# Optimization experiments

Hardware: AMD Instinct MI355X
Metric: run time of the kernel (lower is better)

Reference implementation:

```python
import jax, jax.numpy as jnp
import numpy as np

B, L, D = 8, 512, 256


def hard_sigmoid(x):
    # Keras 1.x default inner_activation for LSTM gates
    return jnp.clip(0.2 * x + 0.5, 0.0, 1.0)


def lstm_step(x_t, h, c, W, U, b):
    # gates in Keras order: i, f, g(candidate), o
    z = x_t @ W + h @ U + b  # (B, 4D)
    i, f, g, o = jnp.split(z, 4, axis=-1)
    i = hard_sigmoid(i)
    f = hard_sigmoid(f)
    g = jnp.tanh(g)
    o = hard_sigmoid(o)
    c_new = f * c + i * g
    h_new = o * jnp.tanh(c_new)
    return h_new, c_new


def setup_inputs() -> dict:
    key = jax.random.key(0)
    ks = jax.random.split(key, 10)
    s = 1.0 / np.sqrt(D)
    x = jax.random.normal(ks[0], (B, L, D), dtype=jnp.float32)
    W_r = jax.random.normal(ks[1], (D, 4 * D), dtype=jnp.float32) * s
    U_r = jax.random.normal(ks[2], (D, 4 * D), dtype=jnp.float32) * s
    b_r = jnp.zeros((4 * D,), dtype=jnp.float32)
    W_w = jax.random.normal(ks[3], (D, 4 * D), dtype=jnp.float32) * s
    U_w = jax.random.normal(ks[4], (D, 4 * D), dtype=jnp.float32) * s
    b_w = jnp.zeros((4 * D,), dtype=jnp.float32)
    W_c = jax.random.normal(ks[5], (2 * D, D), dtype=jnp.float32) * s
    b_c = jnp.zeros((D,), dtype=jnp.float32)
    return {"x": x, "W_r": W_r, "U_r": U_r, "b_r": b_r,
            "W_w": W_w, "U_w": U_w, "b_w": b_w, "W_c": W_c, "b_c": b_c}


def reference(x, W_r, U_r, b_r, W_w, U_w, b_w, W_c, b_c):
    Bb, Ll, Dd = x.shape
    h0 = jnp.zeros((Bb, Dd), dtype=x.dtype)

    # --- reader LSTM (return_sequences=True), eq. 1 ---
    def reader_step(carry, x_t):
        h, c = carry
        h, c = lstm_step(x_t, h, c, W_r, U_r, b_r)
        return (h, c), h

    _, o_seq = jax.lax.scan(reader_step, (h0, h0), jnp.swapaxes(x, 0, 1))  # (L, B, D)

    # --- compose-and-write loop, eqs. 2-6; mem_0 = x ---
    def write_step(carry, o_t):
        mem, h, c = carry  # mem: (B, L, D)
        z = jax.nn.softmax(jnp.einsum('bd,bld->bl', o_t, mem), axis=-1)  # (B, L)
        m_rt = jnp.einsum('bl,bld->bd', z, mem)                           # (B, D)
        c_t = jnp.concatenate([o_t, m_rt], axis=-1) @ W_c + b_c          # linear composer
        h_new, c_new = lstm_step(c_t, h, c, W_w, U_w, b_w)
        mem_new = mem * (1.0 - z[..., None]) + h_new[:, None, :] * z[..., None]
        return (mem_new, h_new, c_new), h_new

    (_, _, _), h_seq = jax.lax.scan(write_step, (x, h0, h0), o_seq)
    # return_mode == 'last_output'
    return h_seq[-1]
```

## Files before the change

kernel.cpp:

```cpp
#include <hip/hip_runtime.h>
#include <math.h>

#define BB 8
#define LL 512
#define DD 256
#define NG4 1024
#define WGB 32
#define WR 16
#define WU 8
#define MLD 264

typedef __attribute__((ext_vector_type(4))) float f32x4;
typedef __attribute__((ext_vector_type(2))) unsigned u32x2;
typedef __attribute__((ext_vector_type(4))) unsigned u32x4;

static const size_t OFF_XW    = 0;
static const size_t OFF_F     = OFF_XW + (size_t)BB*LL*NG4;
static const size_t OFF_BMW   = OFF_F + (size_t)DD*NG4;
static const size_t OFF_B2    = OFF_BMW + (size_t)DD*NG4;
static const size_t OFF_HRT   = OFF_B2 + NG4;
static const size_t OFF_HWT   = OFF_HRT + (size_t)2*BB*DD*2;
static const size_t OFF_RHOT  = OFF_HWT + (size_t)BB*DD*2;
static const size_t OFF_CHUNK = OFF_RHOT + (size_t)BB*WGB*2;
static const size_t OFF_PM    = OFF_CHUNK + (size_t)BB*WGB*4;
static const size_t TOTAL_WS  = OFF_PM + (size_t)BB*WGB*DD;

__device__ __forceinline__ float hsig(float x) {
    return fminf(fmaxf(0.2f*x + 0.5f, 0.0f), 1.0f);
}

__device__ __forceinline__ void st_coh(float* p, float v) {
    __hip_atomic_store(p, v, __ATOMIC_RELAXED, __HIP_MEMORY_SCOPE_AGENT);
}
__device__ __forceinline__ void st_pair(unsigned* p, float v, unsigned tag) {
    u32x2 d; d[0] = __float_as_uint(v); d[1] = tag;
    asm volatile("global_store_dwordx2 %0, %1, off sc0 sc1" :: "v"(p), "v"(d) : "memory");
}
__device__ __forceinline__ u32x2 ld_pair(const unsigned* p) {
    u32x2 r;
    asm volatile("global_load_dwordx2 %0, %1, off sc0 sc1\n\ts_waitcnt vmcnt(0)"
                 : "=&v"(r) : "v"(p) : "memory");
    return r;
}
__device__ __forceinline__ float poll_pair(const unsigned* p, unsigned tag) {
    for (;;) {
        u32x2 r = ld_pair(p);
        if (r[1] >= tag) return __uint_as_float(r[0]);
    }
}
__device__ __forceinline__ u32x4 ld_chunk(const unsigned* p) {
    u32x4 r;
    asm volatile("global_load_dwordx4 %0, %1, off sc0 sc1\n\ts_waitcnt vmcnt(0)"
                 : "=&v"(r) : "v"(p) : "memory");
    return r;
}
__device__ __forceinline__ void ld_pm8(
    const f32x4* p0, const f32x4* p1, const f32x4* p2, const f32x4* p3,
    const f32x4* p4, const f32x4* p5, const f32x4* p6, const f32x4* p7,
    f32x4& a0, f32x4& a1, f32x4& a2, f32x4& a3,
    f32x4& a4, f32x4& a5, f32x4& a6, f32x4& a7)
{
    asm volatile(
        "global_load_dwordx4 %0, %8, off sc0 sc1\n\t"
        "global_load_dwordx4 %1, %9, off sc0 sc1\n\t"
        "global_load_dwordx4 %2, %10, off sc0 sc1\n\t"
        "global_load_dwordx4 %3, %11, off sc0 sc1\n\t"
        "global_load_dwordx4 %4, %12, off sc0 sc1\n\t"
        "global_load_dwordx4 %5, %13, off sc0 sc1\n\t"
        "global_load_dwordx4 %6, %14, off sc0 sc1\n\t"
        "global_load_dwordx4 %7, %15, off sc0 sc1\n\t"
        "s_waitcnt vmcnt(0)"
        : "=&v"(a0), "=&v"(a1), "=&v"(a2), "=&v"(a3),
          "=&v"(a4), "=&v"(a5), "=&v"(a6), "=&v"(a7)
        : "v"(p0), "v"(p1), "v"(p2), "v"(p3),
          "v"(p4), "v"(p5), "v"(p6), "v"(p7)
        : "memory");
}

template<int TM, int TN, int TK>
__global__ void __launch_bounds__(256) gemm_nn(
    const float* __restrict__ A, int lda,
    const float* __restrict__ Bmat, int ldb,
    const float* __restrict__ bias,
    float* __restrict__ C, int ldc,
    int M, int N, int K)
{
    __shared__ float As[TK][TM];
    __shared__ float Bs[TK][TN];
    const int m0 = blockIdx.y * TM, n0 = blockIdx.x * TN;
    const int tid = threadIdx.x;
    const int tx = tid % (TN/4);
    const int ty = tid / (TN/4);
    float acc[4][4] = {};
    for (int k0 = 0; k0 < K; k0 += TK) {
        {
            const int e = tid*4;
            const int m = e / TK, k = e % TK;
            const float4 v = *reinterpret_cast<const float4*>(&A[(size_t)(m0+m)*lda + k0 + k]);
            As[k+0][m] = v.x; As[k+1][m] = v.y; As[k+2][m] = v.z; As[k+3][m] = v.w;
        }
        {
            const int e = tid*4;
            const int k = e / TN, n = e % TN;
            const float4 v = *reinterpret_cast<const float4*>(&Bmat[(size_t)(k0+k)*ldb + n0 + n]);
            Bs[k][n+0] = v.x; Bs[k][n+1] = v.y; Bs[k][n+2] = v.z; Bs[k][n+3] = v.w;
        }
        __syncthreads();
        #pragma unroll
        for (int kk = 0; kk < TK; ++kk) {
            float a[4], bv[4];
            #pragma unroll
            for (int i = 0; i < 4; ++i) a[i] = As[kk][ty*4+i];
            #pragma unroll
            for (int j = 0; j < 4; ++j) bv[j] = Bs[kk][tx*4+j];
            #pragma unroll
            for (int i = 0; i < 4; ++i)
                #pragma unroll
                for (int j = 0; j < 4; ++j) acc[i][j] += a[i]*bv[j];
        }
        __syncthreads();
    }
    #pragma unroll
    for (int i = 0; i < 4; ++i) {
        const int m = m0 + ty*4 + i;
        #pragma unroll
        for (int j = 0; j < 4; ++j) {
            const int n = n0 + tx*4 + j;
            C[(size_t)m*ldc + n] = acc[i][j] + (bias ? bias[n] : 0.0f);
        }
    }
}

__global__ void __launch_bounds__(256) b2_kernel(
    const float* __restrict__ bc, const float* __restrict__ Ww,
    const float* __restrict__ bw, float* __restrict__ B2)
{
    const int n = blockIdx.x*256 + threadIdx.x;
    float a = bw[n];
    for (int k = 0; k < DD; ++k) a += bc[k]*Ww[(size_t)k*NG4 + n];
    B2[n] = a;
}

__global__ void __launch_bounds__(256) fused_kernel(
    const float* __restrict__ XW, const float* __restrict__ Fw,
    const float* __restrict__ Bm, const float* __restrict__ B2,
    const float* __restrict__ Ur, const float* __restrict__ Uw,
    const float* __restrict__ x,
    unsigned* __restrict__ HRT, unsigned* __restrict__ HWT,
    unsigned* __restrict__ RHOT, unsigned* __restrict__ CHUNK,
    float* __restrict__ PM, float* __restrict__ out)
{
    extern __shared__ float sm[];
    float* Urs  = sm;
    float* Uws  = Urs + 8192;
    float* Fs   = Uws + 8192;
    float* Bms  = Fs + 8192;
    float* mems = Bms + 8192;
    float* hr2  = mems + WR*MLD;
    float* hw   = hr2 + 512;
    float* ms   = hw + 256;
    float* zredR= ms + 256;
    float* zredW= zredR + 256;
    float* red4 = zredW + 256;
    float* xws  = red4 + 1024;
    float* b2s  = xws + 32;
    float* zrs  = b2s + 32;
    float* zws  = zrs + 32;
    float* fwS  = zws + 32;
    float* d1   = fwS + 32;
    float* zp   = d1 + 16;
    float* esx  = zp + 16;
    float* wv   = esx + 16;
    float* cr   = wv + 16;
    float* cw   = cr + 8;
    float* misc = cw + 8;

    const int b   = (int)blockIdx.x & 7;
    const int wg  = (int)blockIdx.x >> 3;
    const int tid = threadIdx.x;
    const int R0  = wg*WR;
    const int U0  = wg*WU;
    const int gc32 = (tid>>3)*DD + U0 + (tid&7);

    for (int it = 0; it < 32; ++it) {
        const int e = it*256 + tid;
        const int k = e >> 5, cl = e & 31;
        const int gc = (cl>>3)*DD + U0 + (cl&7);
        Urs[k*32+cl] = Ur[(size_t)k*NG4 + gc];
        Uws[k*32+cl] = Uw[(size_t)k*NG4 + gc];
        Fs [k*32+cl] = Fw[(size_t)k*NG4 + gc];
        Bms[k*32+cl] = Bm[(size_t)k*NG4 + gc];
    }
    if (tid < 32) b2s[tid] = B2[gc32];
    for (int r = 0; r < WR; ++r)
        mems[r*MLD + tid] = x[((size_t)b*LL + R0 + r)*DD + tid];
    {
        const size_t base = (size_t)b*LL*NG4;
        const float zi = XW[base + tid];
        const float zg = XW[base + 512 + tid];
        const float zo = XW[base + 768 + tid];
        const float c0 = hsig(zi)*tanhf(zg);
        hr2[tid] = hsig(zo)*tanhf(c0);
        hr2[256 + tid] = 0.f;
        if (tid >= U0 && tid < U0+WU) cr[tid-U0] = c0;
    }
    if (tid < 16) { zp[tid] = 0.f; d1[tid] = 0.f; esx[tid] = 0.f; }
    if (tid < 8)  cw[tid] = 0.f;
    if (tid < 4)  misc[tid] = 0.f;
    __syncthreads();

    for (int s = 0; s <= LL; ++s) {
        const bool doW = (s >= 1);
        float* hrN_s = hr2 + (s&1)*256;
        float* hrO_s = hr2 + ((s+1)&1)*256;

        if (s <= LL-2 && tid < 32)
            xws[tid] = XW[((size_t)b*LL + s + 1)*NG4 + gc32];

        float hw_r = 0.f, rho_r = 0.f;
        if (s >= 2) {
            hw_r = poll_pair(HWT + 2*((size_t)b*DD + tid), (unsigned)(s-1));
            if (tid < 32)
                rho_r = poll_pair(RHOT + 2*(b*WGB + tid), (unsigned)(s-1));
        }
        hw[tid] = hw_r;
        __syncthreads();

        float ck_m = 0.f, ck_s = 0.f;
        if (tid < 32) {
            float d2 = rho_r;
            #pragma unroll
            for (int off = 16; off; off >>= 1) d2 += __shfl_xor(d2, off, 32);
            if (doW && tid < 16) {
                const float zpv = zp[tid];
                const float sc  = (1.f - zpv)*d1[tid] + zpv*d2;
                float m = sc;
                #pragma unroll
                for (int off = 8; off; off >>= 1) m = fmaxf(m, __shfl_xor(m, off, 16));
                const float e = __expf(sc - m);
                esx[tid] = e;
                wv[tid]  = e*(1.f - zpv);
                float sum = e, bp = e*zpv;
                #pragma unroll
                for (int off = 8; off; off >>= 1) {
                    sum += __shfl_xor(sum, off, 16);
                    bp  += __shfl_xor(bp,  off, 16);
                }
                if (tid == 0) { misc[2] = bp; ck_m = m; ck_s = sum; }
            }
        }
        __syncthreads();

        if (doW) {
            float p = misc[2]*hw_r;
            #pragma unroll
            for (int r = 0; r < WR; ++r) p += wv[r]*mems[r*MLD + tid];
            st_coh(&PM[((size_t)b*WGB + wg)*DD + tid], p);
        }
        asm volatile("s_waitcnt vmcnt(0)" ::: "memory");
        __syncthreads();
        if (doW && tid == 0) {
            u32x4 d; d[0] = __float_as_uint(ck_m); d[1] = __float_as_uint(ck_s);
            d[2] = (unsigned)s; d[3] = 0u;
            unsigned* cp = CHUNK + 4*(b*WGB + wg);
            asm volatile("global_store_dwordx4 %0, %1, off sc0 sc1" :: "v"(cp), "v"(d) : "memory");
        }
        if (s >= 2) {
            #pragma unroll
            for (int r = 0; r < WR; ++r) {
                const float z = zp[r];
                float* mp = &mems[r*MLD + tid];
                *mp = *mp*(1.f - z) + hw_r*z;
            }
        }
        if (doW) {
            const int kc = tid >> 5, cl = tid & 31, k0 = kc*32;
            float a = 0.f;
            #pragma unroll 8
            for (int k = k0; k < k0+32; ++k)
                a += hw[k]*Uws[k*32+cl] + hrO_s[k]*Fs[k*32+cl];
            zredW[tid] = a;
        }

        float hrN_r = 0.f;
        if (s >= 1 && s <= LL-1)
            hrN_r = poll_pair(HRT + 2*(((size_t)(s&1)*BB + b)*DD + tid), (unsigned)s);
        float pmx_r = 0.f, ps_r = 0.f;
        if (doW && tid < 32) {
            const unsigned* cp = CHUNK + 4*(b*WGB + tid);
            u32x4 ck;
            do { ck = ld_chunk(cp); } while (ck[2] < (unsigned)s);
            pmx_r = __uint_as_float(ck[0]); ps_r = __uint_as_float(ck[1]);
        }
        if (s >= 1 && s <= LL-1) hrN_s[tid] = hrN_r;
        __syncthreads();

        f32x4 a0={},a1={},a2={},a3={},a4={},a5={},a6={},a7={};
        const int w0 = tid >> 6, dq = tid & 63;
        if (doW) {
            const float* pmb = PM + (size_t)b*WGB*DD;
            ld_pm8((const f32x4*)(pmb + (w0+ 0)*DD) + dq, (const f32x4*)(pmb + (w0+ 4)*DD) + dq,
                   (const f32x4*)(pmb + (w0+ 8)*DD) + dq, (const f32x4*)(pmb + (w0+12)*DD) + dq,
                   (const f32x4*)(pmb + (w0+16)*DD) + dq, (const f32x4*)(pmb + (w0+20)*DD) + dq,
                   (const f32x4*)(pmb + (w0+24)*DD) + dq, (const f32x4*)(pmb + (w0+28)*DD) + dq,
                   a0,a1,a2,a3,a4,a5,a6,a7);
        }
        if (doW && tid < 32) {
            float g = pmx_r;
            #pragma unroll
            for (int off = 16; off; off >>= 1) g = fmaxf(g, __shfl_xor(g, off, 32));
            const float fw = __expf(pmx_r - g);
            float S = ps_r*fw;
            #pragma unroll
            for (int off = 16; off; off >>= 1) S += __shfl_xor(S, off, 32);
            fwS[tid] = fw;
            if (tid == 0)  misc[1] = 1.f/S;
            if (tid == wg) misc[0] = fw/S;
        }
        if (s <= LL-2) {
            const int kc = tid >> 5, cl = tid & 31, k0 = kc*32;
            float a = 0.f;
            #pragma unroll 8
            for (int k = k0; k < k0+32; ++k) a += hrN_s[k]*Urs[k*32+cl];
            zredR[tid] = a;
        }
        __syncthreads();

        if (doW) {
            f32x4 acc = a0*fwS[w0];
            acc += a1*fwS[w0+4];  acc += a2*fwS[w0+8];
            acc += a3*fwS[w0+12]; acc += a4*fwS[w0+16];
            acc += a5*fwS[w0+20]; acc += a6*fwS[w0+24];
            acc += a7*fwS[w0+28];
            *(f32x4*)(red4 + w0*DD + dq*4) = acc;
        }
        __syncthreads();
        if (doW) {
            ms[tid] = (red4[tid] + red4[DD+tid] + red4[2*DD+tid] + red4[3*DD+tid]) * misc[1];
            if (tid < 16) zp[tid] = esx[tid]*misc[0];
        }
        __syncthreads();
        if (doW) {
            const int kc = tid >> 5, cl = tid & 31, k0 = kc*32;
            float a = zredW[tid];
            #pragma unroll 8
            for (int k = k0; k < k0+32; ++k) a += ms[k]*Bms[k*32+cl];
            zredW[tid] = a;
        }
        __syncthreads();
        if (tid < 32) {
            if (doW) {
                float z = b2s[tid];
                #pragma unroll
                for (int q = 0; q < 8; ++q) z += zredW[q*32 + tid];
                zws[tid] = z;
            }
            if (s <= LL-2) {
                float z = xws[tid];
                #pragma unroll
                for (int q = 0; q < 8; ++q) z += zredR[q*32 + tid];
                zrs[tid] = z;
            }
        }
        __syncthreads();

        if (doW && tid < 8) {
            const float ig = hsig(zws[tid]);
            const float fg = hsig(zws[8+tid]);
            const float gg = tanhf(zws[16+tid]);
            const float og = hsig(zws[24+tid]);
            const float c  = fg*cw[tid] + ig*gg;
            cw[tid] = c;
            const float h = og*tanhf(c);
            st_pair(HWT + 2*((size_t)b*DD + U0 + tid), h, (unsigned)s);
            if (s < LL) {
                float rr = h * hrN_s[U0 + tid];
                rr += __shfl_down(rr, 4, 8);
                rr += __shfl_down(rr, 2, 8);
                rr += __shfl_down(rr, 1, 8);
                if (tid == 0) st_pair(RHOT + 2*(b*WGB + wg), rr, (unsigned)s);
            }
            if (s == LL) out[b*DD + U0 + tid] = h;
        }
        if (s <= LL-2 && tid < 8) {
            const float ig = hsig(zrs[tid]);
            const float fg = hsig(zrs[8+tid]);
            const float gg = tanhf(zrs[16+tid]);
            const float og = hsig(zrs[24+tid]);
            const float c  = fg*cr[tid] + ig*gg;
            cr[tid] = c;
            st_pair(HRT + 2*(((size_t)((s+1)&1)*BB + b)*DD + U0 + tid),
                    og*tanhf(c), (unsigned)(s+1));
        }
        if (s < LL) {
            const int r = tid >> 4, j = tid & 15;
            float a = 0.f;
            const float* mrow = mems + r*MLD;
            #pragma unroll 4
            for (int d = j; d < DD; d += 16) a += hrN_s[d]*mrow[d];
            #pragma unroll
            for (int off = 8; off; off >>= 1) a += __shfl_down(a, off, 16);
            if (j == 0) d1[r] = a;
        }
    }
}

extern "C" void kernel_launch(void* const* d_in, const int* in_sizes, int n_in,
                              void* d_out, int out_size, void* d_ws, size_t ws_size,
                              hipStream_t stream) {
    const float* x   = (const float*)d_in[0];
    const float* W_r = (const float*)d_in[1];
    const float* U_r = (const float*)d_in[2];
    const float* b_r = (const float*)d_in[3];
    const float* W_w = (const float*)d_in[4];
    const float* U_w = (const float*)d_in[5];
    const float* b_w = (const float*)d_in[6];
    const float* W_c = (const float*)d_in[7];
    const float* b_c = (const float*)d_in[8];
    (void)in_sizes; (void)n_in;

    if (ws_size < TOTAL_WS * sizeof(float)) return;

    float* ws   = (float*)d_ws;
    float* XW   = ws + OFF_XW;
    float* Fmat = ws + OFF_F;
    float* Bmw  = ws + OFF_BMW;
    float* B2   = ws + OFF_B2;
    unsigned* HRT   = (unsigned*)(ws + OFF_HRT);
    unsigned* HWT   = (unsigned*)(ws + OFF_HWT);
    unsigned* RHOT  = (unsigned*)(ws + OFF_RHOT);
    unsigned* CHUNK = (unsigned*)(ws + OFF_CHUNK);
    float* PM   = ws + OFF_PM;

    const int FUSED_LDS = 39800 * 4;
    hipFuncSetAttribute((const void*)fused_kernel, hipFuncAttributeMaxDynamicSharedMemorySize, FUSED_LDS);

    hipMemsetAsync(HRT, 0, (OFF_PM - OFF_HRT)*sizeof(float), stream);

    dim3 blk(256);
    gemm_nn<64,64,16><<<dim3(NG4/64, (BB*LL)/64), blk, 0, stream>>>(
        x, DD, W_r, NG4, b_r, XW, NG4, BB*LL, NG4, DD);
    gemm_nn<64,64,16><<<dim3(NG4/64, DD/64), blk, 0, stream>>>(
        W_c, DD, W_w, NG4, nullptr, Fmat, NG4, DD, NG4, DD);
    gemm_nn<64,64,16><<<dim3(NG4/64, DD/64), blk, 0, stream>>>(
        W_c + (size_t)DD*DD, DD, W_w, NG4, nullptr, Bmw, NG4, DD, NG4, DD);
    b2_kernel<<<dim3(NG4/256), blk, 0, stream>>>(b_c, W_w, b_w, B2);
    fused_kernel<<<dim3(BB*WGB), blk, FUSED_LDS, stream>>>(
        XW, Fmat, Bmw, B2, U_r, U_w, x, HRT, HWT, RHOT, CHUNK, PM, (float*)d_out);
}
```

Baseline: 3.784 ms.

## Tag partial-memory vectors per element to drop a barrier and reorder HW polling

Each partial memory-read value now goes out as a (value, step tag) pair, so consumers poll the tags directly and the producer no longer needs a vmcnt wait and barrier before publishing its chunk record. The hw-dependent term (bp·hw) is moved out of the per-workgroup partial into the consumer, using a bp value carried in the chunk record. That lets the HWT poll move later, overlapping the wait with the partial computation, and HWT is double-buffered by step parity. The cost is twice the traffic for partial reads, spin loops over 16 vector loads, and an extra barrier at the end of each step.

```diff
diff --git a/kernel.cpp b/kernel.cpp
--- a/kernel.cpp
+++ b/kernel.cpp
@@ -20,18 +20,15 @@
 static const size_t OFF_B2    = OFF_BMW + (size_t)DD*NG4;
 static const size_t OFF_HRT   = OFF_B2 + NG4;
 static const size_t OFF_HWT   = OFF_HRT + (size_t)2*BB*DD*2;
-static const size_t OFF_RHOT  = OFF_HWT + (size_t)BB*DD*2;
+static const size_t OFF_RHOT  = OFF_HWT + (size_t)2*BB*DD*2;
 static const size_t OFF_CHUNK = OFF_RHOT + (size_t)BB*WGB*2;
-static const size_t OFF_PM    = OFF_CHUNK + (size_t)BB*WGB*4;
-static const size_t TOTAL_WS  = OFF_PM + (size_t)BB*WGB*DD;
+static const size_t OFF_PMT   = OFF_CHUNK + (size_t)BB*WGB*4;
+static const size_t TOTAL_WS  = OFF_PMT + (size_t)BB*WGB*DD*2;
 
 __device__ __forceinline__ float hsig(float x) {
     return fminf(fmaxf(0.2f*x + 0.5f, 0.0f), 1.0f);
 }
 
-__device__ __forceinline__ void st_coh(float* p, float v) {
-    __hip_atomic_store(p, v, __ATOMIC_RELAXED, __HIP_MEMORY_SCOPE_AGENT);
-}
 __device__ __forceinline__ void st_pair(unsigned* p, float v, unsigned tag) {
     u32x2 d; d[0] = __float_as_uint(v); d[1] = tag;
     asm volatile("global_store_dwordx2 %0, %1, off sc0 sc1" :: "v"(p), "v"(d) : "memory");
@@ -54,26 +51,39 @@
                  : "=&v"(r) : "v"(p) : "memory");
     return r;
 }
-__device__ __forceinline__ void ld_pm8(
-    const f32x4* p0, const f32x4* p1, const f32x4* p2, const f32x4* p3,
-    const f32x4* p4, const f32x4* p5, const f32x4* p6, const f32x4* p7,
-    f32x4& a0, f32x4& a1, f32x4& a2, f32x4& a3,
-    f32x4& a4, f32x4& a5, f32x4& a6, f32x4& a7)
+
+__device__ __forceinline__ void ld_pmt16(
+    const unsigned* q0, const unsigned* q1, const unsigned* q2, const unsigned* q3,
+    const unsigned* q4, const unsigned* q5, const unsigned* q6, const unsigned* q7,
+    u32x4& A0, u32x4& B0, u32x4& A1, u32x4& B1,
+    u32x4& A2, u32x4& B2, u32x4& A3, u32x4& B3,
+    u32x4& A4, u32x4& B4, u32x4& A5, u32x4& B5,
+    u32x4& A6, u32x4& B6, u32x4& A7, u32x4& B7)
 {
     asm volatile(
-        "global_load_dwordx4 %0, %8, off sc0 sc1\n\t"
-        "global_load_dwordx4 %1, %9, off sc0 sc1\n\t"
-        "global_load_dwordx4 %2, %10, off sc0 sc1\n\t"
-        "global_load_dwordx4 %3, %11, off sc0 sc1\n\t"
-        "global_load_dwordx4 %4, %12, off sc0 sc1\n\t"
-        "global_load_dwordx4 %5, %13, off sc0 sc1\n\t"
-        "global_load_dwordx4 %6, %14, off sc0 sc1\n\t"
-        "global_load_dwordx4 %7, %15, off sc0 sc1\n\t"
+        "global_load_dwordx4 %0, %16, off sc0 sc1\n\t"
+        "global_load_dwordx4 %1, %16, off offset:16 sc0 sc1\n\t"
+        "global_load_dwordx4 %2, %17, off sc0 sc1\n\t"
+        "global_load_dwordx4 %3, %17, off offset:16 sc0 sc1\n\t"
+        "global_load_dwordx4 %4, %18, off sc0 sc1\n\t"
+        "global_load_dwordx4 %5, %18, off offset:16 sc0 sc1\n\t"
+        "global_load_dwordx4 %6, %19, off sc0 sc1\n\t"
+        "global_load_dwordx4 %7, %19, off offset:16 sc0 sc1\n\t"
+        "global_load_dwordx4 %8, %20, off sc0 sc1\n\t"
+        "global_load_dwordx4 %9, %20, off offset:16 sc0 sc1\n\t"
+        "global_load_dwordx4 %10, %21, off sc0 sc1\n\t"
+        "global_load_dwordx4 %11, %21, off offset:16 sc0 sc1\n\t"
+        "global_load_dwordx4 %12, %22, off sc0 sc1\n\t"
+        "global_load_dwordx4 %13, %22, off offset:16 sc0 sc1\n\t"
+        "global_load_dwordx4 %14, %23, off sc0 sc1\n\t"
+        "global_load_dwordx4 %15, %23, off offset:16 sc0 sc1\n\t"
         "s_waitcnt vmcnt(0)"
-        : "=&v"(a0), "=&v"(a1), "=&v"(a2), "=&v"(a3),
-          "=&v"(a4), "=&v"(a5), "=&v"(a6), "=&v"(a7)
-        : "v"(p0), "v"(p1), "v"(p2), "v"(p3),
-          "v"(p4), "v"(p5), "v"(p6), "v"(p7)
+        : "=&v"(A0), "=&v"(B0), "=&v"(A1), "=&v"(B1),
+          "=&v"(A2), "=&v"(B2), "=&v"(A3), "=&v"(B3),
+          "=&v"(A4), "=&v"(B4), "=&v"(A5), "=&v"(B5),
+          "=&v"(A6), "=&v"(B6), "=&v"(A7), "=&v"(B7)
+        : "v"(q0), "v"(q1), "v"(q2), "v"(q3),
+          "v"(q4), "v"(q5), "v"(q6), "v"(q7)
         : "memory");
 }
 
@@ -148,7 +158,7 @@
     const float* __restrict__ x,
     unsigned* __restrict__ HRT, unsigned* __restrict__ HWT,
     unsigned* __restrict__ RHOT, unsigned* __restrict__ CHUNK,
-    float* __restrict__ PM, float* __restrict__ out)
+    unsigned* __restrict__ PMT, float* __restrict__ out)
 {
     extern __shared__ float sm[];
     float* Urs  = sm;
@@ -211,22 +221,14 @@
 
     for (int s = 0; s <= LL; ++s) {
         const bool doW = (s >= 1);
+        const unsigned us = (unsigned)s;
         float* hrN_s = hr2 + (s&1)*256;
         float* hrO_s = hr2 + ((s+1)&1)*256;
 
         if (s <= LL-2 && tid < 32)
             xws[tid] = XW[((size_t)b*LL + s + 1)*NG4 + gc32];
-
-        float hw_r = 0.f, rho_r = 0.f;
-        if (s >= 2) {
-            hw_r = poll_pair(HWT + 2*((size_t)b*DD + tid), (unsigned)(s-1));
-            if (tid < 32)
-                rho_r = poll_pair(RHOT + 2*(b*WGB + tid), (unsigned)(s-1));
-        }
-        hw[tid] = hw_r;
-        __syncthreads();
-
-        float ck_m = 0.f, ck_s = 0.f;
+        float rho_r = 0.f;
+        if (s >= 2 && tid < 32) rho_r = poll_pair(RHOT + 2*(b*WGB + tid), us - 1u);
         if (tid < 32) {
             float d2 = rho_r;
             #pragma unroll
@@ -246,25 +248,29 @@
                     sum += __shfl_xor(sum, off, 16);
                     bp  += __shfl_xor(bp,  off, 16);
                 }
-                if (tid == 0) { misc[2] = bp; ck_m = m; ck_s = sum; }
+                if (tid == 0) {
+                    u32x4 d; d[0] = __float_as_uint(m); d[1] = __float_as_uint(sum);
+                    d[2] = __float_as_uint(bp); d[3] = us;
+                    unsigned* cp = CHUNK + 4*(b*WGB + wg);
+                    asm volatile("global_store_dwordx4 %0, %1, off sc0 sc1"
+                                 :: "v"(cp), "v"(d) : "memory");
+                }
             }
         }
         __syncthreads();
 
         if (doW) {
-            float p = misc[2]*hw_r;
+            float p = 0.f;
             #pragma unroll
             for (int r = 0; r < WR; ++r) p += wv[r]*mems[r*MLD + tid];
-            st_coh(&PM[((size_t)b*WGB + wg)*DD + tid], p);
-        }
-        asm volatile("s_waitcnt vmcnt(0)" ::: "memory");
-        __syncthreads();
-        if (doW && tid == 0) {
-            u32x4 d; d[0] = __float_as_uint(ck_m); d[1] = __float_as_uint(ck_s);
-            d[2] = (unsigned)s; d[3] = 0u;
-            unsigned* cp = CHUNK + 4*(b*WGB + wg);
-            asm volatile("global_store_dwordx4 %0, %1, off sc0 sc1" :: "v"(cp), "v"(d) : "memory");
-        }
+            st_pair(PMT + 2*(((size_t)b*WGB + wg)*DD + tid), p, us);
+        }
+
+        float hw_r = 0.f;
+        if (s >= 2)
+            hw_r = poll_pair(HWT + 2*((((size_t)((s-1)&1))*BB + b)*DD + tid), us - 1u);
+        hw[tid] = hw_r;
+        __syncthreads();
         if (s >= 2) {
             #pragma unroll
             for (int r = 0; r < WR; ++r) {
@@ -284,39 +290,31 @@
 
         float hrN_r = 0.f;
         if (s >= 1 && s <= LL-1)
-            hrN_r = poll_pair(HRT + 2*(((size_t)(s&1)*BB + b)*DD + tid), (unsigned)s);
-        float pmx_r = 0.f, ps_r = 0.f;
+            hrN_r = poll_pair(HRT + 2*((((size_t)(s&1))*BB + b)*DD + tid), us);
         if (doW && tid < 32) {
             const unsigned* cp = CHUNK + 4*(b*WGB + tid);
             u32x4 ck;
-            do { ck = ld_chunk(cp); } while (ck[2] < (unsigned)s);
-            pmx_r = __uint_as_float(ck[0]); ps_r = __uint_as_float(ck[1]);
-        }
-        if (s >= 1 && s <= LL-1) hrN_s[tid] = hrN_r;
-        __syncthreads();
-
-        f32x4 a0={},a1={},a2={},a3={},a4={},a5={},a6={},a7={};
-        const int w0 = tid >> 6, dq = tid & 63;
-        if (doW) {
-            const float* pmb = PM + (size_t)b*WGB*DD;
-            ld_pm8((const f32x4*)(pmb + (w0+ 0)*DD) + dq, (const f32x4*)(pmb + (w0+ 4)*DD) + dq,
-                   (const f32x4*)(pmb + (w0+ 8)*DD) + dq, (const f32x4*)(pmb + (w0+12)*DD) + dq,
-                   (const f32x4*)(pmb + (w0+16)*DD) + dq, (const f32x4*)(pmb + (w0+20)*DD) + dq,
-                   (const f32x4*)(pmb + (w0+24)*DD) + dq, (const f32x4*)(pmb + (w0+28)*DD) + dq,
-                   a0,a1,a2,a3,a4,a5,a6,a7);
-        }
-        if (doW && tid < 32) {
+            do { ck = ld_chunk(cp); } while (ck[3] < us);
+            const float pmx_r = __uint_as_float(ck[0]);
+            const float ps_r  = __uint_as_float(ck[1]);
+            const float bt_r  = __uint_as_float(ck[2]);
             float g = pmx_r;
             #pragma unroll
             for (int off = 16; off; off >>= 1) g = fmaxf(g, __shfl_xor(g, off, 32));
             const float fw = __expf(pmx_r - g);
-            float S = ps_r*fw;
-            #pragma unroll
-            for (int off = 16; off; off >>= 1) S += __shfl_xor(S, off, 32);
+            float S = ps_r*fw, gp = bt_r*fw;
+            #pragma unroll
+            for (int off = 16; off; off >>= 1) {
+                S  += __shfl_xor(S,  off, 32);
+                gp += __shfl_xor(gp, off, 32);
+            }
             fwS[tid] = fw;
-            if (tid == 0)  misc[1] = 1.f/S;
+            if (tid == 0)  { misc[1] = 1.f/S; misc[3] = gp; }
             if (tid == wg) misc[0] = fw/S;
         }
+        if (s >= 1 && s <= LL-1) hrN_s[tid] = hrN_r;
+        __syncthreads();
+
         if (s <= LL-2) {
             const int kc = tid >> 5, cl = tid & 31, k0 = kc*32;
             float a = 0.f;
@@ -324,19 +322,57 @@
             for (int k = k0; k < k0+32; ++k) a += hrN_s[k]*Urs[k*32+cl];
             zredR[tid] = a;
         }
-        __syncthreads();
-
+        const int w0 = tid >> 6, dq = tid & 63;
         if (doW) {
-            f32x4 acc = a0*fwS[w0];
-            acc += a1*fwS[w0+4];  acc += a2*fwS[w0+8];
-            acc += a3*fwS[w0+12]; acc += a4*fwS[w0+16];
-            acc += a5*fwS[w0+20]; acc += a6*fwS[w0+24];
-            acc += a7*fwS[w0+28];
+            const unsigned* pmtb = PMT + 2*(size_t)b*WGB*DD;
+            const unsigned* q0 = pmtb + 2*((w0+ 0)*DD + dq*4);
+            const unsigned* q1 = pmtb + 2*((w0+ 4)*DD + dq*4);
+            const unsigned* q2 = pmtb + 2*((w0+ 8)*DD + dq*4);
+            const unsigned* q3 = pmtb + 2*((w0+12)*DD + dq*4);
+            const unsigned* q4 = pmtb + 2*((w0+16)*DD + dq*4);
+            const unsigned* q5 = pmtb + 2*((w0+20)*DD + dq*4);
+            const unsigned* q6 = pmtb + 2*((w0+24)*DD + dq*4);
+            const unsigned* q7 = pmtb + 2*((w0+28)*DD + dq*4);
+            u32x4 A0,B0,A1,B1,A2,B2,A3,B3,A4,B4,A5,B5,A6,B6,A7,B7;
+            for (;;) {
+                ld_pmt16(q0,q1,q2,q3,q4,q5,q6,q7,
+                         A0,B0,A1,B1,A2,B2,A3,B3,A4,B4,A5,B5,A6,B6,A7,B7);
+                unsigned t0 = min(min(A0[1],A0[3]), min(B0[1],B0[3]));
+                unsigned t1 = min(min(A1[1],A1[3]), min(B1[1],B1[3]));
+                unsigned t2 = min(min(A2[1],A2[3]), min(B2[1],B2[3]));
+                unsigned t3 = min(min(A3[1],A3[3]), min(B3[1],B3[3]));
+                unsigned t4 = min(min(A4[1],A4[3]), min(B4[1],B4[3]));
+                unsigned t5 = min(min(A5[1],A5[3]), min(B5[1],B5[3]));
+                unsigned t6 = min(min(A6[1],A6[3]), min(B6[1],B6[3]));
+                unsigned t7 = min(min(A7[1],A7[3]), min(B7[1],B7[3]));
+                unsigned t = min(min(min(t0,t1),min(t2,t3)), min(min(t4,t5),min(t6,t7)));
+                if (t >= us) break;
+            }
+            const float f0 = fwS[w0+ 0], f1 = fwS[w0+ 4], f2 = fwS[w0+ 8], f3 = fwS[w0+12];
+            const float f4 = fwS[w0+16], f5 = fwS[w0+20], f6 = fwS[w0+24], f7 = fwS[w0+28];
+            f32x4 acc;
+            acc[0] = f0*__uint_as_float(A0[0]) + f1*__uint_as_float(A1[0])
+                   + f2*__uint_as_float(A2[0]) + f3*__uint_as_float(A3[0])
+                   + f4*__uint_as_float(A4[0]) + f5*__uint_as_float(A5[0])
+                   + f6*__uint_as_float(A6[0]) + f7*__uint_as_float(A7[0]);
+            acc[1] = f0*__uint_as_float(A0[2]) + f1*__uint_as_float(A1[2])
+                   + f2*__uint_as_float(A2[2]) + f3*__uint_as_float(A3[2])
+                   + f4*__uint_as_float(A4[2]) + f5*__uint_as_float(A5[2])
+                   + f6*__uint_as_float(A6[2]) + f7*__uint_as_float(A7[2]);
+            acc[2] = f0*__uint_as_float(B0[0]) + f1*__uint_as_float(B1[0])
+                   + f2*__uint_as_float(B2[0]) + f3*__uint_as_float(B3[0])
+                   + f4*__uint_as_float(B4[0]) + f5*__uint_as_float(B5[0])
+                   + f6*__uint_as_float(B6[0]) + f7*__uint_as_float(B7[0]);
+            acc[3] = f0*__uint_as_float(B0[2]) + f1*__uint_as_float(B1[2])
+                   + f2*__uint_as_float(B2[2]) + f3*__uint_as_float(B3[2])
+                   + f4*__uint_as_float(B4[2]) + f5*__uint_as_float(B5[2])
+                   + f6*__uint_as_float(B6[2]) + f7*__uint_as_float(B7[2]);
             *(f32x4*)(red4 + w0*DD + dq*4) = acc;
         }
         __syncthreads();
         if (doW) {
-            ms[tid] = (red4[tid] + red4[DD+tid] + red4[2*DD+tid] + red4[3*DD+tid]) * misc[1];
+            ms[tid] = (red4[tid] + red4[DD+tid] + red4[2*DD+tid] + red4[3*DD+tid]
+                       + misc[3]*hw[tid]) * misc[1];
             if (tid < 16) zp[tid] = esx[tid]*misc[0];
         }
         __syncthreads();
@@ -372,13 +408,13 @@
             const float c  = fg*cw[tid] + ig*gg;
             cw[tid] = c;
             const float h = og*tanhf(c);
-            st_pair(HWT + 2*((size_t)b*DD + U0 + tid), h, (unsigned)s);
+            st_pair(HWT + 2*((((size_t)(s&1))*BB + b)*DD + U0 + tid), h, us);
             if (s < LL) {
                 float rr = h * hrN_s[U0 + tid];
                 rr += __shfl_down(rr, 4, 8);
                 rr += __shfl_down(rr, 2, 8);
                 rr += __shfl_down(rr, 1, 8);
-                if (tid == 0) st_pair(RHOT + 2*(b*WGB + wg), rr, (unsigned)s);
+                if (tid == 0) st_pair(RHOT + 2*(b*WGB + wg), rr, us);
             }
             if (s == LL) out[b*DD + U0 + tid] = h;
         }
@@ -389,8 +425,8 @@
             const float og = hsig(zrs[24+tid]);
             const float c  = fg*cr[tid] + ig*gg;
             cr[tid] = c;
-            st_pair(HRT + 2*(((size_t)((s+1)&1)*BB + b)*DD + U0 + tid),
-                    og*tanhf(c), (unsigned)(s+1));
+            st_pair(HRT + 2*((((size_t)((s+1)&1))*BB + b)*DD + U0 + tid),
+                    og*tanhf(c), us + 1u);
         }
         if (s < LL) {
             const int r = tid >> 4, j = tid & 15;
@@ -402,6 +438,7 @@
             for (int off = 8; off; off >>= 1) a += __shfl_down(a, off, 16);
             if (j == 0) d1[r] = a;
         }
+        __syncthreads();
     }
 }
 
@@ -430,12 +467,12 @@
     unsigned* HWT   = (unsigned*)(ws + OFF_HWT);
     unsigned* RHOT  = (unsigned*)(ws + OFF_RHOT);
     unsigned* CHUNK = (unsigned*)(ws + OFF_CHUNK);
-    float* PM   = ws + OFF_PM;
+    unsigned* PMT   = (unsigned*)(ws + OFF_PMT);
 
     const int FUSED_LDS = 39800 * 4;
     hipFuncSetAttribute((const void*)fused_kernel, hipFuncAttributeMaxDynamicSharedMemorySize, FUSED_LDS);
 
-    hipMemsetAsync(HRT, 0, (OFF_PM - OFF_HRT)*sizeof(float), stream);
+    hipMemsetAsync(HRT, 0, (TOTAL_WS - OFF_HRT)*sizeof(float), stream);
 
     dim3 blk(256);
     gemm_nn<64,64,16><<<dim3(NG4/64, (BB*LL)/64), blk, 0, stream>>>(
@@ -446,5 +483,5 @@
         W_c + (size_t)DD*DD, DD, W_w, NG4, nullptr, Bmw, NG4, DD, NG4, DD);
     b2_kernel<<<dim3(NG4/256), blk, 0, stream>>>(b_c, W_w, b_w, B2);
     fused_kernel<<<dim3(BB*WGB), blk, FUSED_LDS, stream>>>(
-        XW, Fmat, Bmw, B2, U_r, U_w, x, HRT, HWT, RHOT, CHUNK, PM, (float*)d_out);
-}
+        XW, Fmat, Bmw, B2, U_r, U_w, x, HRT, HWT, RHOT, CHUNK, PMT, (float*)d_out);
+}
```

Result: slower. 4.042 ms (+6.8%).

## Restructure cross-workgroup polling into batched loads and a flag-gated partial-memory exchange

Applied to the files above, without the earlier changes.

Issues the HW, HR and RHO polls together in one asm sequence so their global latencies overlap, and moves the HR read earlier in the step. Replaces the 16-byte chunk record, which was written after a separate barrier, with a sum pair written early and a flag pair that carries the running max and the step tag. Once the flag is seen, the partial memory vectors and the sum are loaded together. Barriers are moved around to shorten the critical path, with the risk of subtle memory-ordering bugs between the sum store and the flag.

```diff
diff --git a/kernel.cpp b/kernel.cpp
--- a/kernel.cpp
+++ b/kernel.cpp
@@ -21,8 +21,9 @@
 static const size_t OFF_HRT   = OFF_B2 + NG4;
 static const size_t OFF_HWT   = OFF_HRT + (size_t)2*BB*DD*2;
 static const size_t OFF_RHOT  = OFF_HWT + (size_t)BB*DD*2;
-static const size_t OFF_CHUNK = OFF_RHOT + (size_t)BB*WGB*2;
-static const size_t OFF_PM    = OFF_CHUNK + (size_t)BB*WGB*4;
+static const size_t OFF_CH2   = OFF_RHOT + (size_t)BB*WGB*2;
+static const size_t OFF_FLG   = OFF_CH2 + (size_t)BB*WGB*2;
+static const size_t OFF_PM    = OFF_FLG + (size_t)BB*WGB*2;
 static const size_t TOTAL_WS  = OFF_PM + (size_t)BB*WGB*DD;
 
 __device__ __forceinline__ float hsig(float x) {
@@ -47,34 +48,6 @@
         u32x2 r = ld_pair(p);
         if (r[1] >= tag) return __uint_as_float(r[0]);
     }
-}
-__device__ __forceinline__ u32x4 ld_chunk(const unsigned* p) {
-    u32x4 r;
-    asm volatile("global_load_dwordx4 %0, %1, off sc0 sc1\n\ts_waitcnt vmcnt(0)"
-                 : "=&v"(r) : "v"(p) : "memory");
-    return r;
-}
-__device__ __forceinline__ void ld_pm8(
-    const f32x4* p0, const f32x4* p1, const f32x4* p2, const f32x4* p3,
-    const f32x4* p4, const f32x4* p5, const f32x4* p6, const f32x4* p7,
-    f32x4& a0, f32x4& a1, f32x4& a2, f32x4& a3,
-    f32x4& a4, f32x4& a5, f32x4& a6, f32x4& a7)
-{
-    asm volatile(
-        "global_load_dwordx4 %0, %8, off sc0 sc1\n\t"
-        "global_load_dwordx4 %1, %9, off sc0 sc1\n\t"
-        "global_load_dwordx4 %2, %10, off sc0 sc1\n\t"
-        "global_load_dwordx4 %3, %11, off sc0 sc1\n\t"
-        "global_load_dwordx4 %4, %12, off sc0 sc1\n\t"
-        "global_load_dwordx4 %5, %13, off sc0 sc1\n\t"
-        "global_load_dwordx4 %6, %14, off sc0 sc1\n\t"
-        "global_load_dwordx4 %7, %15, off sc0 sc1\n\t"
-        "s_waitcnt vmcnt(0)"
-        : "=&v"(a0), "=&v"(a1), "=&v"(a2), "=&v"(a3),
-          "=&v"(a4), "=&v"(a5), "=&v"(a6), "=&v"(a7)
-        : "v"(p0), "v"(p1), "v"(p2), "v"(p3),
-          "v"(p4), "v"(p5), "v"(p6), "v"(p7)
-        : "memory");
 }
 
 template<int TM, int TN, int TK>
@@ -147,8 +120,9 @@
     const float* __restrict__ Ur, const float* __restrict__ Uw,
     const float* __restrict__ x,
     unsigned* __restrict__ HRT, unsigned* __restrict__ HWT,
-    unsigned* __restrict__ RHOT, unsigned* __restrict__ CHUNK,
-    float* __restrict__ PM, float* __restrict__ out)
+    unsigned* __restrict__ RHOT, unsigned* __restrict__ CH2,
+    unsigned* __restrict__ FLG, float* __restrict__ PMf,
+    float* __restrict__ out)
 {
     extern __shared__ float sm[];
     float* Urs  = sm;
@@ -211,22 +185,43 @@
 
     for (int s = 0; s <= LL; ++s) {
         const bool doW = (s >= 1);
+        const unsigned us = (unsigned)s;
         float* hrN_s = hr2 + (s&1)*256;
         float* hrO_s = hr2 + ((s+1)&1)*256;
 
+        const unsigned* phw = HWT + 2*((size_t)b*DD + tid);
+        const unsigned* phr = HRT + 2*((((size_t)(s&1))*BB + b)*DD + tid);
+        const unsigned* prh = RHOT + 2*(b*WGB + (tid & 31));
+        const unsigned long long trho = (s >= 2) ? ((unsigned long long)(s-1) << 32) : 0ull;
+        unsigned long long hwp, hrp, rrp;
+        asm volatile(
+            "global_load_dwordx2 %[hw], %[phw], off sc0 sc1\n\t"
+            "global_load_dwordx2 %[hr], %[phr], off sc0 sc1\n\t"
+            "1:\n\t"
+            "global_load_dwordx2 %[rr], %[prh], off sc0 sc1\n\t"
+            "s_waitcnt vmcnt(0)\n\t"
+            "v_cmp_gt_u64 vcc, %[tr], %[rr]\n\t"
+            "s_cbranch_vccnz 1b"
+            : [hw]"=&v"(hwp), [hr]"=&v"(hrp), [rr]"=&v"(rrp)
+            : [phw]"v"(phw), [phr]"v"(phr), [prh]"v"(prh), [tr]"s"(trho)
+            : "vcc", "memory");
+
+        const float rho_r = (s >= 2) ? __uint_as_float((unsigned)rrp) : 0.f;
+        float hw_r = 0.f;
+        if (s >= 2) {
+            hw_r = ((unsigned)(hwp >> 32) >= us - 1u)
+                 ? __uint_as_float((unsigned)hwp) : poll_pair(phw, us - 1u);
+        }
+        if (s >= 1 && s <= LL-1) {
+            const float hrN_r = ((unsigned)(hrp >> 32) >= us)
+                 ? __uint_as_float((unsigned)hrp) : poll_pair(phr, us);
+            hrN_s[tid] = hrN_r;
+        }
+        hw[tid] = hw_r;
         if (s <= LL-2 && tid < 32)
             xws[tid] = XW[((size_t)b*LL + s + 1)*NG4 + gc32];
 
-        float hw_r = 0.f, rho_r = 0.f;
-        if (s >= 2) {
-            hw_r = poll_pair(HWT + 2*((size_t)b*DD + tid), (unsigned)(s-1));
-            if (tid < 32)
-                rho_r = poll_pair(RHOT + 2*(b*WGB + tid), (unsigned)(s-1));
-        }
-        hw[tid] = hw_r;
-        __syncthreads();
-
-        float ck_m = 0.f, ck_s = 0.f;
+        float ck_m = 0.f;
         if (tid < 32) {
             float d2 = rho_r;
             #pragma unroll
@@ -246,7 +241,11 @@
                     sum += __shfl_xor(sum, off, 16);
                     bp  += __shfl_xor(bp,  off, 16);
                 }
-                if (tid == 0) { misc[2] = bp; ck_m = m; ck_s = sum; }
+                if (tid == 0) {
+                    misc[2] = bp;
+                    ck_m = m;
+                    st_pair(CH2 + 2*(b*WGB + wg), sum, 0u);
+                }
             }
         }
         __syncthreads();
@@ -255,16 +254,9 @@
             float p = misc[2]*hw_r;
             #pragma unroll
             for (int r = 0; r < WR; ++r) p += wv[r]*mems[r*MLD + tid];
-            st_coh(&PM[((size_t)b*WGB + wg)*DD + tid], p);
-        }
-        asm volatile("s_waitcnt vmcnt(0)" ::: "memory");
-        __syncthreads();
-        if (doW && tid == 0) {
-            u32x4 d; d[0] = __float_as_uint(ck_m); d[1] = __float_as_uint(ck_s);
-            d[2] = (unsigned)s; d[3] = 0u;
-            unsigned* cp = CHUNK + 4*(b*WGB + wg);
-            asm volatile("global_store_dwordx4 %0, %1, off sc0 sc1" :: "v"(cp), "v"(d) : "memory");
-        }
+            st_coh(&PMf[((size_t)b*WGB + wg)*DD + tid], p);
+        }
+
         if (s >= 2) {
             #pragma unroll
             for (int r = 0; r < WR; ++r) {
@@ -281,29 +273,56 @@
                 a += hw[k]*Uws[k*32+cl] + hrO_s[k]*Fs[k*32+cl];
             zredW[tid] = a;
         }
-
-        float hrN_r = 0.f;
-        if (s >= 1 && s <= LL-1)
-            hrN_r = poll_pair(HRT + 2*(((size_t)(s&1)*BB + b)*DD + tid), (unsigned)s);
+        asm volatile("s_waitcnt vmcnt(0)" ::: "memory");
+        __syncthreads();
+        if (doW && tid == 0)
+            st_pair(FLG + 2*(b*WGB + wg), ck_m, us);
+
         float pmx_r = 0.f, ps_r = 0.f;
-        if (doW && tid < 32) {
-            const unsigned* cp = CHUNK + 4*(b*WGB + tid);
-            u32x4 ck;
-            do { ck = ld_chunk(cp); } while (ck[2] < (unsigned)s);
-            pmx_r = __uint_as_float(ck[0]); ps_r = __uint_as_float(ck[1]);
-        }
-        if (s >= 1 && s <= LL-1) hrN_s[tid] = hrN_r;
-        __syncthreads();
-
         f32x4 a0={},a1={},a2={},a3={},a4={},a5={},a6={},a7={};
         const int w0 = tid >> 6, dq = tid & 63;
         if (doW) {
-            const float* pmb = PM + (size_t)b*WGB*DD;
-            ld_pm8((const f32x4*)(pmb + (w0+ 0)*DD) + dq, (const f32x4*)(pmb + (w0+ 4)*DD) + dq,
-                   (const f32x4*)(pmb + (w0+ 8)*DD) + dq, (const f32x4*)(pmb + (w0+12)*DD) + dq,
-                   (const f32x4*)(pmb + (w0+16)*DD) + dq, (const f32x4*)(pmb + (w0+20)*DD) + dq,
-                   (const f32x4*)(pmb + (w0+24)*DD) + dq, (const f32x4*)(pmb + (w0+28)*DD) + dq,
-                   a0,a1,a2,a3,a4,a5,a6,a7);
+            const unsigned* pfl = FLG + 2*(b*WGB + (tid & 31));
+            const unsigned long long tf = ((unsigned long long)us) << 32;
+            unsigned long long flgp;
+            asm volatile(
+                "1:\n\t"
+                "global_load_dwordx2 %[f], %[pf], off sc0 sc1\n\t"
+                "s_waitcnt vmcnt(0)\n\t"
+                "v_cmp_gt_u64 vcc, %[t], %[f]\n\t"
+                "s_cbranch_vccnz 1b"
+                : [f]"=&v"(flgp)
+                : [pf]"v"(pfl), [t]"s"(tf)
+                : "vcc", "memory");
+            pmx_r = __uint_as_float((unsigned)flgp);
+            const float* pmb = PMf + (size_t)b*WGB*DD;
+            const unsigned* pc2 = CH2 + 2*(b*WGB + (tid & 31));
+            unsigned long long c2p;
+            asm volatile(
+                "global_load_dwordx2 %[c], %[pc], off sc0 sc1\n\t"
+                "global_load_dwordx4 %[a0], %[q0], off sc0 sc1\n\t"
+                "global_load_dwordx4 %[a1], %[q1], off sc0 sc1\n\t"
+                "global_load_dwordx4 %[a2], %[q2], off sc0 sc1\n\t"
+                "global_load_dwordx4 %[a3], %[q3], off sc0 sc1\n\t"
+                "global_load_dwordx4 %[a4], %[q4], off sc0 sc1\n\t"
+                "global_load_dwordx4 %[a5], %[q5], off sc0 sc1\n\t"
+                "global_load_dwordx4 %[a6], %[q6], off sc0 sc1\n\t"
+                "global_load_dwordx4 %[a7], %[q7], off sc0 sc1\n\t"
+                "s_waitcnt vmcnt(0)"
+                : [c]"=&v"(c2p),
+                  [a0]"=&v"(a0), [a1]"=&v"(a1), [a2]"=&v"(a2), [a3]"=&v"(a3),
+                  [a4]"=&v"(a4), [a5]"=&v"(a5), [a6]"=&v"(a6), [a7]"=&v"(a7)
+                : [pc]"v"(pc2),
+                  [q0]"v"((const f32x4*)(pmb + (w0+ 0)*DD) + dq),
+                  [q1]"v"((const f32x4*)(pmb + (w0+ 4)*DD) + dq),
+                  [q2]"v"((const f32x4*)(pmb + (w0+ 8)*DD) + dq),
+                  [q3]"v"((const f32x4*)(pmb + (w0+12)*DD) + dq),
+                  [q4]"v"((const f32x4*)(pmb + (w0+16)*DD) + dq),
+                  [q5]"v"((const f32x4*)(pmb + (w0+20)*DD) + dq),
+                  [q6]"v"((const f32x4*)(pmb + (w0+24)*DD) + dq),
+                  [q7]"v"((const f32x4*)(pmb + (w0+28)*DD) + dq)
+                : "memory");
+            ps_r = __uint_as_float((unsigned)c2p);
         }
         if (doW && tid < 32) {
             float g = pmx_r;
@@ -317,6 +336,8 @@
             if (tid == 0)  misc[1] = 1.f/S;
             if (tid == wg) misc[0] = fw/S;
         }
+        __syncthreads();
+
         if (s <= LL-2) {
             const int kc = tid >> 5, cl = tid & 31, k0 = kc*32;
             float a = 0.f;
@@ -324,8 +345,6 @@
             for (int k = k0; k < k0+32; ++k) a += hrN_s[k]*Urs[k*32+cl];
             zredR[tid] = a;
         }
-        __syncthreads();
-
         if (doW) {
             f32x4 acc = a0*fwS[w0];
             acc += a1*fwS[w0+4];  acc += a2*fwS[w0+8];
@@ -372,13 +391,13 @@
             const float c  = fg*cw[tid] + ig*gg;
             cw[tid] = c;
             const float h = og*tanhf(c);
-            st_pair(HWT + 2*((size_t)b*DD + U0 + tid), h, (unsigned)s);
+            st_pair(HWT + 2*((size_t)b*DD + U0 + tid), h, us);
             if (s < LL) {
                 float rr = h * hrN_s[U0 + tid];
                 rr += __shfl_down(rr, 4, 8);
                 rr += __shfl_down(rr, 2, 8);
                 rr += __shfl_down(rr, 1, 8);
-                if (tid == 0) st_pair(RHOT + 2*(b*WGB + wg), rr, (unsigned)s);
+                if (tid == 0) st_pair(RHOT + 2*(b*WGB + wg), rr, us);
             }
             if (s == LL) out[b*DD + U0 + tid] = h;
         }
@@ -389,8 +408,8 @@
             const float og = hsig(zrs[24+tid]);
             const float c  = fg*cr[tid] + ig*gg;
             cr[tid] = c;
-            st_pair(HRT + 2*(((size_t)((s+1)&1)*BB + b)*DD + U0 + tid),
-                    og*tanhf(c), (unsigned)(s+1));
+            st_pair(HRT + 2*((((size_t)((s+1)&1))*BB + b)*DD + U0 + tid),
+                    og*tanhf(c), us + 1u);
         }
         if (s < LL) {
             const int r = tid >> 4, j = tid & 15;
@@ -402,6 +421,7 @@
             for (int off = 8; off; off >>= 1) a += __shfl_down(a, off, 16);
             if (j == 0) d1[r] = a;
         }
+        __syncthreads();
     }
 }
 
@@ -426,11 +446,12 @@
     float* Fmat = ws + OFF_F;
     float* Bmw  = ws + OFF_BMW;
     float* B2   = ws + OFF_B2;
-    unsigned* HRT   = (unsigned*)(ws + OFF_HRT);
-    unsigned* HWT   = (unsigned*)(ws + OFF_HWT);
-    unsigned* RHOT  = (unsigned*)(ws + OFF_RHOT);
-    unsigned* CHUNK = (unsigned*)(ws + OFF_CHUNK);
-    float* PM   = ws + OFF_PM;
+    unsigned* HRT  = (unsigned*)(ws + OFF_HRT);
+    unsigned* HWT  = (unsigned*)(ws + OFF_HWT);
+    unsigned* RHOT = (unsigned*)(ws + OFF_RHOT);
+    unsigned* CH2  = (unsigned*)(ws + OFF_CH2);
+    unsigned* FLG  = (unsigned*)(ws + OFF_FLG);
+    float* PMf  = ws + OFF_PM;
 
     const int FUSED_LDS = 39800 * 4;
     hipFuncSetAttribute((const void*)fused_kernel, hipFuncAttributeMaxDynamicSharedMemorySize, FUSED_LDS);
@@ -446,5 +467,5 @@
         W_c + (size_t)DD*DD, DD, W_w, NG4, nullptr, Bmw, NG4, DD, NG4, DD);
     b2_kernel<<<dim3(NG4/256), blk, 0, stream>>>(b_c, W_w, b_w, B2);
     fused_kernel<<<dim3(BB*WGB), blk, FUSED_LDS, stream>>>(
-        XW, Fmat, Bmw, B2, U_r, U_w, x, HRT, HWT, RHOT, CHUNK, PM, (float*)d_out);
-}
+        XW, Fmat, Bmw, B2, U_r, U_w, x, HRT, HWT, RHOT, CH2, FLG, PMf, (float*)d_out);
+}
```

After: 4.348 ms. +14.9%, slower.
